# Optimization experiments

Measured on AMD Instinct MI355X. Metric: run time of the kernel, lower is better.

## Reference

```python
import jax, jax.numpy as jnp
import numpy as np
from jax import lax

DN = ('NCHW', 'OIHW', 'NCHW')
DENSITY = 0.1  # fraction of active pillar sites


def conv(x, w, stride=1):
    return lax.conv_general_dilated(x, w, (stride, stride), ((1, 1), (1, 1)), dimension_numbers=DN)


def bn(x, s, t):
    # inference-mode BN folded into per-channel scale/shift
    return x * s[None, :, None, None] + t[None, :, None, None]


def subm(x, w, s, t, mask):
    # submanifold sparse conv == dense conv on zero-filled grid, outputs kept only at active sites
    return bn(conv(x, w), s, t) * mask


def basic_block(x, mask, w, s, t):
    # Sparse2DBasicBlock: relu(bn(conv)) -> bn(conv) -> add identity -> relu
    out = jax.nn.relu(subm(x, w[0], s[0], t[0], mask))
    out = subm(out, w[1], s[1], t[1], mask)
    return jax.nn.relu(out + x)


def downsample_mask(m):
    # regular sparse conv (k=3, s=2, p=1): output active iff any input in window active
    return lax.reduce_window(m, 0.0, lax.max, (1, 1, 3, 3), (1, 1, 2, 2), ((0, 0), (0, 0), (1, 1), (1, 1)))


def down_stage(x, m_in, wd, w, s, t):
    m = downsample_mask(m_in)
    h = jax.nn.relu(bn(conv(x, wd, 2), s[0], t[0]) * m)
    h = basic_block(h, m, w[0:2], s[1:3], t[1:3])
    h = basic_block(h, m, w[2:4], s[3:5], t[3:5])
    return h, m


def forward_all(x, mask, w1, s1, t1, wd2, w2, s2, t2, wd3, w3, s3, t3, wd4, w4, s4, t4, w5, s5, t5):
    x = x * mask
    # conv1: Sparse2DBasicBlockV (conv0 + block) + Sparse2DBasicBlock
    h = jax.nn.relu(subm(x, w1[0], s1[0], t1[0], mask))
    h = basic_block(h, mask, w1[1:3], s1[1:3], t1[1:3])
    x1 = basic_block(h, mask, w1[3:5], s1[3:5], t1[3:5])
    x2, m2 = down_stage(x1, mask, wd2, w2, s2, t2)
    x3, m3 = down_stage(x2, m2, wd3, w3, s3, t3)
    x4, m4 = down_stage(x3, m3, wd4, w4, s4, t4)
    # conv5: dense stage on x_conv4.dense()
    h = jax.nn.relu(bn(conv(x4, w5[0], 2), s5[0], t5[0]))
    h = jax.nn.relu(bn(conv(h, w5[1]), s5[1], t5[1]))
    x5 = jax.nn.relu(bn(conv(h, w5[2]), s5[2], t5[2]))
    return x1, x2, x3, x4, x5


def setup_inputs() -> dict:
    key = jax.random.key(0)
    ks = jax.random.split(key, 16)
    B, C, H, W = 2, 32, 512, 512

    def mkw(k, o, i, n=None):
        shape = (o, i, 3, 3) if n is None else (n, o, i, 3, 3)
        return jax.random.normal(k, shape, jnp.float32) * float(np.sqrt(2.0 / (i * 9)))

    def sb(k, n, c):
        k1, k2 = jax.random.split(k)
        return (1.0 + 0.1 * jax.random.normal(k1, (n, c), jnp.float32),
                0.05 * jax.random.normal(k2, (n, c), jnp.float32))

    x = jax.random.normal(ks[0], (B, C, H, W), jnp.float32)
    mask_p = jax.random.uniform(ks[1], (B, 1, H, W), jnp.float32)
    w1 = mkw(ks[2], 32, 32, 5); s1, t1 = sb(ks[3], 5, 32)
    wd2 = mkw(ks[4], 64, 32); w2 = mkw(ks[5], 64, 64, 4); s2, t2 = sb(ks[6], 5, 64)
    wd3 = mkw(ks[7], 128, 64); w3 = mkw(ks[8], 128, 128, 4); s3, t3 = sb(ks[9], 5, 128)
    wd4 = mkw(ks[10], 256, 128); w4 = mkw(ks[11], 256, 256, 4); s4, t4 = sb(ks[12], 5, 256)
    w5 = mkw(ks[13], 256, 256, 3); s5, t5 = sb(ks[14], 3, 256)
    return dict(x=x, mask_p=mask_p, w1=w1, s1=s1, t1=t1, wd2=wd2, w2=w2, s2=s2, t2=t2,
                wd3=wd3, w3=w3, s3=s3, t3=t3, wd4=wd4, w4=w4, s4=s4, t4=t4,
                w5=w5, s5=s5, t5=t5)


def reference(x, mask_p, w1, s1, t1, wd2, w2, s2, t2, wd3, w3, s3, t3, wd4, w4, s4, t4, w5, s5, t5):
    mask = (mask_p < DENSITY).astype(x.dtype)
    return forward_all(x, mask, w1, s1, t1, wd2, w2, s2, t2, wd3, w3, s3, t3, wd4, w4, s4, t4, w5, s5, t5)
```

## Files before the change

### kernel.cpp

```cpp
#include <hip/hip_runtime.h>

typedef __attribute__((ext_vector_type(8))) _Float16 f16x8;
typedef __attribute__((ext_vector_type(4))) _Float16 f16x4;
typedef __attribute__((ext_vector_type(4))) float f32x4;

__global__ void mask_make(const float* __restrict__ x, const float* __restrict__ mp,
                          float* __restrict__ m, _Float16* __restrict__ x0,
                          int* __restrict__ act, int* __restrict__ cnt,
                          int B, int HW) {
    int i = blockIdx.x * blockDim.x + threadIdx.x;
    const int tid = threadIdx.x;
    const int lane = tid & 63;
    const int wv = tid >> 6;
    bool active = (mp[i] < 0.1f);
    float mv = active ? 1.0f : 0.0f;
    m[i] = mv;
    int b = i / HW, p = i - b * HW;
    const float* xb = x + ((size_t)b * 32) * HW + p;
    _Float16* ob = x0 + (size_t)i * 32;
    #pragma unroll
    for (int c = 0; c < 32; ++c) ob[c] = (_Float16)(xb[(size_t)c * HW] * mv);

    __shared__ int wcnt[4];
    __shared__ int bbase;
    unsigned long long ball = __ballot(active);
    int wtot = __popcll(ball);
    int prefix = __popcll(ball & ((1ull << lane) - 1ull));
    if (lane == 0) wcnt[wv] = wtot;
    __syncthreads();
    if (tid == 0) {
        int s = 0;
        #pragma unroll
        for (int w = 0; w < 4; ++w) { int tv = wcnt[w]; wcnt[w] = s; s += tv; }
        bbase = (s > 0) ? atomicAdd(&cnt[b], s) : 0;
    }
    __syncthreads();
    if (active) act[b * HW + bbase + wcnt[wv] + prefix] = p;
}

__global__ void mask_down(const float* __restrict__ mi, float* __restrict__ mo,
                          int B, int Hi, int Wi, int Ho, int Wo) {
    int i = blockIdx.x * blockDim.x + threadIdx.x;
    if (i >= B * Ho * Wo) return;
    int wo = i % Wo;
    int t = i / Wo;
    int ho = t % Ho;
    int b = t / Ho;
    float v = 0.0f;
    #pragma unroll
    for (int kh = 0; kh < 3; ++kh) {
        int hi = ho * 2 + kh - 1;
        if (hi < 0 || hi >= Hi) continue;
        #pragma unroll
        for (int kw = 0; kw < 3; ++kw) {
            int wi = wo * 2 + kw - 1;
            if (wi < 0 || wi >= Wi) continue;
            v = fmaxf(v, mi[((size_t)b * Hi + hi) * Wi + wi]);
        }
    }
    mo[i] = v;
}

struct WSeg { const float* src; int cin, cout, ck, cum; };
struct WArgs { WSeg seg[23]; int total; };

__global__ void reorder_all(WArgs A, _Float16* __restrict__ rw) {
    int idx = blockIdx.x * 256 + threadIdx.x;
    if (idx >= A.total) return;
    int s = 0;
    #pragma unroll
    for (int k = 1; k < 23; ++k) if (idx >= A.seg[k].cum) s = k;
    WSeg g = A.seg[s];
    int local = idx - g.cum;
    int kk = local % g.ck;
    int t2 = local / g.ck;
    int co = t2 % g.cout;
    int chunk = t2 / g.cout;
    int chunkc = g.cin / g.ck;
    int tap = chunk / chunkc, cc = chunk - tap * chunkc;
    int ci = cc * g.ck + kk;
    rw[g.cum + local] = (_Float16)g.src[((size_t)co * g.cin + ci) * 9 + tap];
}

template<int BM, int BN, int CK>
__global__ __launch_bounds__(256, 4)
void conv_mfma(const _Float16* __restrict__ in, const _Float16* __restrict__ rw,
               const float* __restrict__ s, const float* __restrict__ t,
               const float* __restrict__ mask, const _Float16* __restrict__ res,
               float* __restrict__ out32, _Float16* __restrict__ out16,
               int Cin, int Cout, int Hin, int Win, int Hout, int Wout,
               int TH, int TW, int stride, int relu)
{
    constexpr int WM = (BM >= 64) ? BM / 2 : BM;
    constexpr int WAVES_M = BM / WM;
    constexpr int WAVES_N = 4 / WAVES_M;
    constexpr int WN = BN / WAVES_N;
    constexpr int MR = WM / 16;
    constexpr int NR = WN / 16;
    constexpr int KH = CK / 32;
    constexpr int ELEMS = (CK * BN) / 256;
    constexpr int NV = ELEMS / 8;
    constexpr int TPP = 256 / BN;
    constexpr int LDST = CK + 8;

    __shared__ _Float16 Bsm[2][BN * LDST];

    const int tid = threadIdx.x;
    const int lane = tid & 63;
    const int wv = tid >> 6;
    const int wm = wv / WAVES_N;
    const int wn = wv % WAVES_N;
    const int row = lane & 15, q = lane >> 4;

    const int tilesX = Wout / TW;
    const int oy0 = (blockIdx.x / tilesX) * TH;
    const int ox0 = (blockIdx.x % tilesX) * TW;
    const int co0 = blockIdx.y * BM;
    const int b = blockIdx.z;

    const int HWin = Hin * Win;
    const int HWo = Hout * Wout;
    const int cicn = Cin >> 5;
    const int cocn = Cout >> 5;
    const int chunkc = Cin / CK;
    const int nIter = 9 * chunkc;

    const int sn = tid / TPP;
    const int kb = (tid % TPP) * ELEMS;
    const int sty = sn / TW;
    const int stx = sn - sty * TW;
    const int soy = oy0 + sty;
    const int sox = ox0 + stx;

    f32x4 acc[MR][NR];
    #pragma unroll
    for (int m = 0; m < MR; ++m)
        #pragma unroll
        for (int n = 0; n < NR; ++n)
            #pragma unroll
            for (int r = 0; r < 4; ++r) acc[m][n][r] = 0.0f;

    auto LOADG = [&](int c, f16x8* dst) {
        int tap = c / chunkc, cc = c - tap * chunkc;
        int iy = soy * stride + (tap / 3) - 1;
        int ix = sox * stride + (tap - (tap / 3) * 3) - 1;
        bool ok = (iy >= 0 && iy < Hin && ix >= 0 && ix < Win);
        size_t pixoff = (size_t)iy * Win + ix;
        #pragma unroll
        for (int i = 0; i < NV; ++i) {
            int k = kb + 8 * i;
            const _Float16* p = in +
                (((size_t)(b * cicn + cc * KH + (k >> 5)) * HWin + pixoff) << 5) + (k & 31);
            dst[i] = ok ? *(const f16x8*)p : f16x8{};
        }
    };
    auto LOADW = [&](int c, f16x8 (&dst)[KH][MR]) {
        #pragma unroll
        for (int m = 0; m < MR; ++m) {
            int co = co0 + wm * WM + m * 16 + row;
            const _Float16* ap = rw + ((size_t)c * Cout + co) * CK + (q << 3);
            #pragma unroll
            for (int h = 0; h < KH; ++h) dst[h][m] = *(const f16x8*)(ap + 32 * h);
        }
    };
    auto WLDS = [&](int buf, const f16x8* v) {
        #pragma unroll
        for (int i = 0; i < NV; ++i)
            *(f16x8*)&Bsm[buf][sn * LDST + kb + 8 * i] = v[i];
    };
    auto DO_CHUNK = [&](const _Float16* bp, f16x8 (&awx)[KH][MR]) {
        f16x8 bh[KH][NR];
        #pragma unroll
        for (int n = 0; n < NR; ++n) {
            int nl = wn * WN + n * 16 + row;
            const _Float16* bb = bp + nl * LDST + (q << 3);
            #pragma unroll
            for (int h = 0; h < KH; ++h) bh[h][n] = *(const f16x8*)(bb + 32 * h);
        }
        #pragma unroll
        for (int h = 0; h < KH; ++h)
            #pragma unroll
            for (int m = 0; m < MR; ++m)
                #pragma unroll
                for (int n = 0; n < NR; ++n)
                    acc[m][n] = __builtin_amdgcn_mfma_f32_16x16x32_f16(awx[h][m], bh[h][n], acc[m][n], 0, 0, 0);
    };

    f16x8 awA[KH][MR], awB[KH][MR];
    f16x8 v[NV];
    LOADG(0, v);
    LOADW(0, awA);
    WLDS(0, v);
    __syncthreads();

    for (int c = 0; c < nIter; c += 2) {
        f16x8 v2[NV];
        bool h1 = (c + 1) < nIter;
        if (h1) { LOADG(c + 1, v2); LOADW(c + 1, awB); }
        DO_CHUNK(&Bsm[0][0], awA);
        if (h1) WLDS(1, v2);
        __syncthreads();
        if (!h1) break;
        f16x8 v3[NV];
        bool h2 = (c + 2) < nIter;
        if (h2) { LOADG(c + 2, v3); LOADW(c + 2, awA); }
        DO_CHUNK(&Bsm[1][0], awB);
        if (h2) WLDS(0, v3);
        __syncthreads();
    }

    int pix[NR]; float mv[NR];
    #pragma unroll
    for (int n = 0; n < NR; ++n) {
        int nl = wn * WN + n * 16 + row;
        int ty = nl / TW, tx = nl - ty * TW;
        pix[n] = (oy0 + ty) * Wout + (ox0 + tx);
        mv[n] = mask ? mask[(size_t)b * HWo + pix[n]] : 1.0f;
    }
    #pragma unroll
    for (int m = 0; m < MR; ++m) {
        int cb = co0 + wm * WM + m * 16 + q * 4;
        float sc[4], sh[4];
        #pragma unroll
        for (int r = 0; r < 4; ++r) { sc[r] = s[cb + r]; sh[r] = t[cb + r]; }
        #pragma unroll
        for (int n = 0; n < NR; ++n) {
            size_t boff = ((size_t)(b * cocn + (cb >> 5)) * HWo + pix[n]) * 32 + (cb & 31);
            float val[4];
            #pragma unroll
            for (int r = 0; r < 4; ++r) val[r] = (acc[m][n][r] * sc[r] + sh[r]) * mv[n];
            if (res) {
                f16x4 rv = *(const f16x4*)&res[boff];
                #pragma unroll
                for (int r = 0; r < 4; ++r) val[r] += (float)rv[r];
            }
            if (relu) {
                #pragma unroll
                for (int r = 0; r < 4; ++r) val[r] = fmaxf(val[r], 0.0f);
            }
            if (out16) {
                f16x4 pk;
                #pragma unroll
                for (int r = 0; r < 4; ++r) pk[r] = (_Float16)val[r];
                *(f16x4*)&out16[boff] = pk;
            }
            if (out32) {
                #pragma unroll
                for (int r = 0; r < 4; ++r)
                    out32[((size_t)b * Cout + cb + r) * HWo + pix[n]] = val[r];
            }
        }
    }
}

__global__ __launch_bounds__(256, 4)
void conv_sparse(const _Float16* __restrict__ in, const _Float16* __restrict__ rw,
                 const float* __restrict__ s, const float* __restrict__ t,
                 const int* __restrict__ act, const int* __restrict__ cnt,
                 const _Float16* __restrict__ res,
                 float* __restrict__ out32, _Float16* __restrict__ out16,
                 int Hin, int Win, int relu)
{
    const int tid = threadIdx.x;
    const int lane = tid & 63;
    const int wv = tid >> 6;
    const int row = lane & 15, q = lane >> 4;
    const int b = blockIdx.z;
    const int HW = Hin * Win;
    const int nb = cnt[b];
    const int base = (blockIdx.x * 4 + wv) * 16;
    if (base >= nb) return;

    const int* actb = act + b * HW;
    const _Float16* inb = in + ((size_t)b * HW << 5);

    int j = base + row;
    bool vn = j < nb;
    int pn = vn ? actb[j] : 0;
    int py = pn / Win, px = pn - py * Win;

    f32x4 acc0, acc1;
    #pragma unroll
    for (int r = 0; r < 4; ++r) { acc0[r] = 0.0f; acc1[r] = 0.0f; }

    #pragma unroll
    for (int c = 0; c < 9; ++c) {
        const int dy = c / 3 - 1, dx = c - (c / 3) * 3 - 1;
        f16x8 a0 = *(const f16x8*)(rw + ((size_t)c * 32 + row) * 32 + (q << 3));
        f16x8 a1 = *(const f16x8*)(rw + ((size_t)c * 32 + 16 + row) * 32 + (q << 3));
        int iy = py + dy, ix = px + dx;
        bool ok = vn && iy >= 0 && iy < Hin && ix >= 0 && ix < Win;
        f16x8 bf = ok ? *(const f16x8*)(inb + ((size_t)(iy * Win + ix) << 5) + (q << 3))
                      : f16x8{};
        acc0 = __builtin_amdgcn_mfma_f32_16x16x32_f16(a0, bf, acc0, 0, 0, 0);
        acc1 = __builtin_amdgcn_mfma_f32_16x16x32_f16(a1, bf, acc1, 0, 0, 0);
    }

    if (!vn) return;
    size_t pbase = ((size_t)b * HW + pn) << 5;
    #pragma unroll
    for (int m = 0; m < 2; ++m) {
        const f32x4& am = m ? acc1 : acc0;
        int cb = m * 16 + q * 4;
        float val[4];
        #pragma unroll
        for (int r = 0; r < 4; ++r) val[r] = am[r] * s[cb + r] + t[cb + r];
        if (res) {
            f16x4 rv = *(const f16x4*)&res[pbase + cb];
            #pragma unroll
            for (int r = 0; r < 4; ++r) val[r] += (float)rv[r];
        }
        if (relu) {
            #pragma unroll
            for (int r = 0; r < 4; ++r) val[r] = fmaxf(val[r], 0.0f);
        }
        f16x4 pk;
        #pragma unroll
        for (int r = 0; r < 4; ++r) pk[r] = (_Float16)val[r];
        *(f16x4*)&out16[pbase + cb] = pk;
        if (out32) {
            #pragma unroll
            for (int r = 0; r < 4; ++r)
                out32[((size_t)(b * 32 + cb + r)) * HW + pn] = val[r];
        }
    }
}

extern "C" void kernel_launch(void* const* d_in, const int* in_sizes, int n_in,
                              void* d_out, int out_size, void* d_ws, size_t ws_size,
                              hipStream_t stream) {
    const int B = 2;

    const float* x      = (const float*)d_in[0];
    const float* mask_p = (const float*)d_in[1];
    const float* w1  = (const float*)d_in[2];
    const float* s1  = (const float*)d_in[3];
    const float* t1  = (const float*)d_in[4];
    const float* wd2 = (const float*)d_in[5];
    const float* w2  = (const float*)d_in[6];
    const float* s2  = (const float*)d_in[7];
    const float* t2  = (const float*)d_in[8];
    const float* wd3 = (const float*)d_in[9];
    const float* w3  = (const float*)d_in[10];
    const float* s3  = (const float*)d_in[11];
    const float* t3  = (const float*)d_in[12];
    const float* wd4 = (const float*)d_in[13];
    const float* w4  = (const float*)d_in[14];
    const float* s4  = (const float*)d_in[15];
    const float* t4  = (const float*)d_in[16];
    const float* w5  = (const float*)d_in[17];
    const float* s5  = (const float*)d_in[18];
    const float* t5  = (const float*)d_in[19];

    float* x1o = (float*)d_out;
    float* x2o = x1o + 16777216;
    float* x3o = x2o + 8388608;
    float* x4o = x3o + 4194304;
    float* x5o = x4o + 2097152;

    _Float16* rwbase = (_Float16*)d_ws;
    float* m1 = (float*)d_ws + 2649600;
    float* m2 = m1 + 524288;
    float* m3 = m2 + 131072;
    float* m4 = m3 + 32768;
    int* act  = (int*)(m4 + 8192);
    int* cnt  = act + 524288;
    _Float16* P = (_Float16*)(cnt + 32);
    _Float16* Q = P + 16777216;
    _Float16* R = Q + 16777216;

    WArgs wa;
    int cum = 0, si = 0;
    const _Float16* rp[23];
    auto addseg = [&](const float* src, int cin, int cout, int ck) {
        wa.seg[si].src = src; wa.seg[si].cin = cin; wa.seg[si].cout = cout;
        wa.seg[si].ck = ck; wa.seg[si].cum = cum;
        rp[si] = rwbase + cum;
        cum += cout * cin * 9; si++;
    };
    for (int i = 0; i < 5; ++i) addseg(w1 + (size_t)i * 9216, 32, 32, 32);
    addseg(wd2, 32, 64, 32);
    for (int i = 0; i < 4; ++i) addseg(w2 + (size_t)i * 36864, 64, 64, 64);
    addseg(wd3, 64, 128, 64);
    for (int i = 0; i < 4; ++i) addseg(w3 + (size_t)i * 147456, 128, 128, 64);
    addseg(wd4, 128, 256, 64);
    for (int i = 0; i < 4; ++i) addseg(w4 + (size_t)i * 589824, 256, 256, 64);
    for (int i = 0; i < 3; ++i) addseg(w5 + (size_t)i * 589824, 256, 256, 64);
    wa.total = cum;
    reorder_all<<<(cum + 255) / 256, 256, 0, stream>>>(wa, rwbase);

    hipMemsetAsync(cnt, 0, 2 * sizeof(int), stream);
    hipMemsetAsync(Q, 0, 16777216 * sizeof(_Float16), stream);
    hipMemsetAsync(R, 0, 16777216 * sizeof(_Float16), stream);
    hipMemsetAsync(x1o, 0, 16777216 * sizeof(float), stream);

    {
        int n = B * 512 * 512;
        mask_make<<<(n + 255) / 256, 256, 0, stream>>>(x, mask_p, m1, P, act, cnt, B, 512 * 512);
        mask_down<<<(B * 256 * 256 + 255) / 256, 256, 0, stream>>>(m1, m2, B, 512, 512, 256, 256);
        mask_down<<<(B * 128 * 128 + 255) / 256, 256, 0, stream>>>(m2, m3, B, 256, 256, 128, 128);
        mask_down<<<(B * 64 * 64 + 255) / 256, 256, 0, stream>>>(m3, m4, B, 128, 128, 64, 64);
    }

    auto conv = [&](const _Float16* in, const _Float16* rwp, const float* sp, const float* tp,
                    const float* mk, const _Float16* rs, float* o32, _Float16* o16,
                    int Cin, int Cout, int Hin, int Win, int stride, int CK) {
        int Hout = Hin / stride, Wout = Win / stride, HWo = Hout * Wout;
        int TW = (Wout < 64) ? Wout : 64;
        int TH = 64 / TW;
        dim3 grid(HWo / 64, Cout / 64, B);
        if (CK == 32)
            conv_mfma<64, 64, 32><<<grid, 256, 0, stream>>>(in, rwp, sp, tp, mk, rs, o32, o16,
                Cin, Cout, Hin, Win, Hout, Wout, TH, TW, stride, 1);
        else
            conv_mfma<64, 64, 64><<<grid, 256, 0, stream>>>(in, rwp, sp, tp, mk, rs, o32, o16,
                Cin, Cout, Hin, Win, Hout, Wout, TH, TW, stride, 1);
    };
    auto sconv = [&](const _Float16* in, const _Float16* rwp, const float* sp, const float* tp,
                     const _Float16* rs, float* o32, _Float16* o16) {
        dim3 grid(1024, 1, B);
        conv_sparse<<<grid, 256, 0, stream>>>(in, rwp, sp, tp, act, cnt, rs, o32, o16, 512, 512, 1);
    };

    sconv(P, rp[0], s1 + 0,   t1 + 0,   nullptr, nullptr, Q);
    sconv(Q, rp[1], s1 + 32,  t1 + 32,  nullptr, nullptr, R);
    sconv(R, rp[2], s1 + 64,  t1 + 64,  Q,       nullptr, P);
    sconv(P, rp[3], s1 + 96,  t1 + 96,  nullptr, nullptr, Q);
    sconv(Q, rp[4], s1 + 128, t1 + 128, P,       x1o,     R);

    conv(R, rp[5], s2 + 0,   t2 + 0,   m2, nullptr, nullptr, P, 32, 64, 512, 512, 2, 32);
    conv(P, rp[6], s2 + 64,  t2 + 64,  m2, nullptr, nullptr, Q, 64, 64, 256, 256, 1, 64);
    conv(Q, rp[7], s2 + 128, t2 + 128, m2, P,       nullptr, P, 64, 64, 256, 256, 1, 64);
    conv(P, rp[8], s2 + 192, t2 + 192, m2, nullptr, nullptr, Q, 64, 64, 256, 256, 1, 64);
    conv(Q, rp[9], s2 + 256, t2 + 256, m2, P,       x2o,     P, 64, 64, 256, 256, 1, 64);

    conv(P, rp[10], s3 + 0,   t3 + 0,   m3, nullptr, nullptr, Q, 64, 128, 256, 256, 2, 64);
    conv(Q, rp[11], s3 + 128, t3 + 128, m3, nullptr, nullptr, R, 128, 128, 128, 128, 1, 64);
    conv(R, rp[12], s3 + 256, t3 + 256, m3, Q,       nullptr, Q, 128, 128, 128, 128, 1, 64);
    conv(Q, rp[13], s3 + 384, t3 + 384, m3, nullptr, nullptr, R, 128, 128, 128, 128, 1, 64);
    conv(R, rp[14], s3 + 512, t3 + 512, m3, Q,       x3o,     Q, 128, 128, 128, 128, 1, 64);

    conv(Q, rp[15], s4 + 0,    t4 + 0,    m4, nullptr, nullptr, P, 128, 256, 128, 128, 2, 64);
    conv(P, rp[16], s4 + 256,  t4 + 256,  m4, nullptr, nullptr, R, 256, 256, 64, 64, 1, 64);
    conv(R, rp[17], s4 + 512,  t4 + 512,  m4, P,       nullptr, P, 256, 256, 64, 64, 1, 64);
    conv(P, rp[18], s4 + 768,  t4 + 768,  m4, nullptr, nullptr, R, 256, 256, 64, 64, 1, 64);
    conv(R, rp[19], s4 + 1024, t4 + 1024, m4, P,       x4o,     P, 256, 256, 64, 64, 1, 64);

    conv(P, rp[20], s5 + 0,   t5 + 0,   nullptr, nullptr, nullptr, Q, 256, 256, 64, 64, 2, 64);
    conv(Q, rp[21], s5 + 256, t5 + 256, nullptr, nullptr, nullptr, R, 256, 256, 32, 32, 1, 64);
    conv(R, rp[22], s5 + 512, t5 + 512, nullptr, nullptr, x5o, nullptr, 256, 256, 32, 32, 1, 64);
}
```

Before: 1.087 ms.

## Deepen conv prefetch pipeline, use narrower pixel tiles for deep stages, merge memsets

The dense MFMA conv main loop now prefetches global input two chunks ahead into register buffers and issues the weight loads after each chunk's MFMAs, so memory latency overlaps more compute. Stages 4 and 5 (64x64 and 32x32 grids, 256 channels) use a 64x32 tile instead of 64x64, doubling block count to fill more CUs on small spatial layers. The two scratch-buffer memsets are merged into one, which assumes Q and R are contiguous. The extra register buffers raise VGPR pressure and may reduce occupancy.

```diff
diff --git a/kernel.cpp b/kernel.cpp
--- a/kernel.cpp
+++ b/kernel.cpp
@@ -91,9 +91,8 @@
                int Cin, int Cout, int Hin, int Win, int Hout, int Wout,
                int TH, int TW, int stride, int relu)
 {
-    constexpr int WM = (BM >= 64) ? BM / 2 : BM;
-    constexpr int WAVES_M = BM / WM;
-    constexpr int WAVES_N = 4 / WAVES_M;
+    constexpr int WM = BM / 2;
+    constexpr int WAVES_N = 2;
     constexpr int WN = BN / WAVES_N;
     constexpr int MR = WM / 16;
     constexpr int NR = WN / 16;
@@ -108,8 +107,8 @@
     const int tid = threadIdx.x;
     const int lane = tid & 63;
     const int wv = tid >> 6;
-    const int wm = wv / WAVES_N;
-    const int wn = wv % WAVES_N;
+    const int wm = wv >> 1;
+    const int wn = wv & 1;
     const int row = lane & 15, q = lane >> 4;
 
     const int tilesX = Wout / TW;
@@ -187,25 +186,25 @@
     };
 
     f16x8 awA[KH][MR], awB[KH][MR];
-    f16x8 v[NV];
-    LOADG(0, v);
+    f16x8 vA[NV], vB[NV];
+    LOADG(0, vA);
     LOADW(0, awA);
-    WLDS(0, v);
+    WLDS(0, vA);
+    if (1 < nIter) { LOADG(1, vB); LOADW(1, awB); }
     __syncthreads();
 
     for (int c = 0; c < nIter; c += 2) {
-        f16x8 v2[NV];
-        bool h1 = (c + 1) < nIter;
-        if (h1) { LOADG(c + 1, v2); LOADW(c + 1, awB); }
+        bool n1 = (c + 1) < nIter, n2 = (c + 2) < nIter, n3 = (c + 3) < nIter;
+        if (n2) LOADG(c + 2, vA);
         DO_CHUNK(&Bsm[0][0], awA);
-        if (h1) WLDS(1, v2);
+        if (n2) LOADW(c + 2, awA);
+        if (n1) WLDS(1, vB);
         __syncthreads();
-        if (!h1) break;
-        f16x8 v3[NV];
-        bool h2 = (c + 2) < nIter;
-        if (h2) { LOADG(c + 2, v3); LOADW(c + 2, awA); }
+        if (!n1) break;
+        if (n3) LOADG(c + 3, vB);
         DO_CHUNK(&Bsm[1][0], awB);
-        if (h2) WLDS(0, v3);
+        if (n3) LOADW(c + 3, awB);
+        if (n2) WLDS(0, vA);
         __syncthreads();
     }
 
@@ -390,8 +389,7 @@
     reorder_all<<<(cum + 255) / 256, 256, 0, stream>>>(wa, rwbase);
 
     hipMemsetAsync(cnt, 0, 2 * sizeof(int), stream);
-    hipMemsetAsync(Q, 0, 16777216 * sizeof(_Float16), stream);
-    hipMemsetAsync(R, 0, 16777216 * sizeof(_Float16), stream);
+    hipMemsetAsync(Q, 0, 2 * 16777216 * sizeof(_Float16), stream);
     hipMemsetAsync(x1o, 0, 16777216 * sizeof(float), stream);
 
     {
@@ -404,16 +402,19 @@
 
     auto conv = [&](const _Float16* in, const _Float16* rwp, const float* sp, const float* tp,
                     const float* mk, const _Float16* rs, float* o32, _Float16* o16,
-                    int Cin, int Cout, int Hin, int Win, int stride, int CK) {
+                    int Cin, int Cout, int Hin, int Win, int stride, int CK, int BN) {
         int Hout = Hin / stride, Wout = Win / stride, HWo = Hout * Wout;
-        int TW = (Wout < 64) ? Wout : 64;
-        int TH = 64 / TW;
-        dim3 grid(HWo / 64, Cout / 64, B);
+        int TW = (Wout < BN) ? Wout : BN;
+        int TH = BN / TW;
+        dim3 grid(HWo / BN, Cout / 64, B);
         if (CK == 32)
             conv_mfma<64, 64, 32><<<grid, 256, 0, stream>>>(in, rwp, sp, tp, mk, rs, o32, o16,
                 Cin, Cout, Hin, Win, Hout, Wout, TH, TW, stride, 1);
+        else if (BN == 64)
+            conv_mfma<64, 64, 64><<<grid, 256, 0, stream>>>(in, rwp, sp, tp, mk, rs, o32, o16,
+                Cin, Cout, Hin, Win, Hout, Wout, TH, TW, stride, 1);
         else
-            conv_mfma<64, 64, 64><<<grid, 256, 0, stream>>>(in, rwp, sp, tp, mk, rs, o32, o16,
+            conv_mfma<64, 32, 64><<<grid, 256, 0, stream>>>(in, rwp, sp, tp, mk, rs, o32, o16,
                 Cin, Cout, Hin, Win, Hout, Wout, TH, TW, stride, 1);
     };
     auto sconv = [&](const _Float16* in, const _Float16* rwp, const float* sp, const float* tp,
@@ -428,25 +429,25 @@
     sconv(P, rp[3], s1 + 96,  t1 + 96,  nullptr, nullptr, Q);
     sconv(Q, rp[4], s1 + 128, t1 + 128, P,       x1o,     R);
 
-    conv(R, rp[5], s2 + 0,   t2 + 0,   m2, nullptr, nullptr, P, 32, 64, 512, 512, 2, 32);
-    conv(P, rp[6], s2 + 64,  t2 + 64,  m2, nullptr, nullptr, Q, 64, 64, 256, 256, 1, 64);
-    conv(Q, rp[7], s2 + 128, t2 + 128, m2, P,       nullptr, P, 64, 64, 256, 256, 1, 64);
-    conv(P, rp[8], s2 + 192, t2 + 192, m2, nullptr, nullptr, Q, 64, 64, 256, 256, 1, 64);
-    conv(Q, rp[9], s2 + 256, t2 + 256, m2, P,       x2o,     P, 64, 64, 256, 256, 1, 64);
-
-    conv(P, rp[10], s3 + 0,   t3 + 0,   m3, nullptr, nullptr, Q, 64, 128, 256, 256, 2, 64);
-    conv(Q, rp[11], s3 + 128, t3 + 128, m3, nullptr, nullptr, R, 128, 128, 128, 128, 1, 64);
-    conv(R, rp[12], s3 + 256, t3 + 256, m3, Q,       nullptr, Q, 128, 128, 128, 128, 1, 64);
-    conv(Q, rp[13], s3 + 384, t3 + 384, m3, nullptr, nullptr, R, 128, 128, 128, 128, 1, 64);
-    conv(R, rp[14], s3 + 512, t3 + 512, m3, Q,       x3o,     Q, 128, 128, 128, 128, 1, 64);
-
-    conv(Q, rp[15], s4 + 0,    t4 + 0,    m4, nullptr, nullptr, P, 128, 256, 128, 128, 2, 64);
-    conv(P, rp[16], s4 + 256,  t4 + 256,  m4, nullptr, nullptr, R, 256, 256, 64, 64, 1, 64);
-    conv(R, rp[17], s4 + 512,  t4 + 512,  m4, P,       nullptr, P, 256, 256, 64, 64, 1, 64);
-    conv(P, rp[18], s4 + 768,  t4 + 768,  m4, nullptr, nullptr, R, 256, 256, 64, 64, 1, 64);
-    conv(R, rp[19], s4 + 1024, t4 + 1024, m4, P,       x4o,     P, 256, 256, 64, 64, 1, 64);
-
-    conv(P, rp[20], s5 + 0,   t5 + 0,   nullptr, nullptr, nullptr, Q, 256, 256, 64, 64, 2, 64);
-    conv(Q, rp[21], s5 + 256, t5 + 256, nullptr, nullptr, nullptr, R, 256, 256, 32, 32, 1, 64);
-    conv(R, rp[22], s5 + 512, t5 + 512, nullptr, nullptr, x5o, nullptr, 256, 256, 32, 32, 1, 64);
-}
+    conv(R, rp[5], s2 + 0,   t2 + 0,   m2, nullptr, nullptr, P, 32, 64, 512, 512, 2, 32, 64);
+    conv(P, rp[6], s2 + 64,  t2 + 64,  m2, nullptr, nullptr, Q, 64, 64, 256, 256, 1, 64, 64);
+    conv(Q, rp[7], s2 + 128, t2 + 128, m2, P,       nullptr, P, 64, 64, 256, 256, 1, 64, 64);
+    conv(P, rp[8], s2 + 192, t2 + 192, m2, nullptr, nullptr, Q, 64, 64, 256, 256, 1, 64, 64);
+    conv(Q, rp[9], s2 + 256, t2 + 256, m2, P,       x2o,     P, 64, 64, 256, 256, 1, 64, 64);
+
+    conv(P, rp[10], s3 + 0,   t3 + 0,   m3, nullptr, nullptr, Q, 64, 128, 256, 256, 2, 64, 64);
+    conv(Q, rp[11], s3 + 128, t3 + 128, m3, nullptr, nullptr, R, 128, 128, 128, 128, 1, 64, 64);
+    conv(R, rp[12], s3 + 256, t3 + 256, m3, Q,       nullptr, Q, 128, 128, 128, 128, 1, 64, 64);
+    conv(Q, rp[13], s3 + 384, t3 + 384, m3, nullptr, nullptr, R, 128, 128, 128, 128, 1, 64, 64);
+    conv(R, rp[14], s3 + 512, t3 + 512, m3, Q,       x3o,     Q, 128, 128, 128, 128, 1, 64, 64);
+
+    conv(Q, rp[15], s4 + 0,    t4 + 0,    m4, nullptr, nullptr, P, 128, 256, 128, 128, 2, 64, 32);
+    conv(P, rp[16], s4 + 256,  t4 + 256,  m4, nullptr, nullptr, R, 256, 256, 64, 64, 1, 64, 32);
+    conv(R, rp[17], s4 + 512,  t4 + 512,  m4, P,       nullptr, P, 256, 256, 64, 64, 1, 64, 32);
+    conv(P, rp[18], s4 + 768,  t4 + 768,  m4, nullptr, nullptr, R, 256, 256, 64, 64, 1, 64, 32);
+    conv(R, rp[19], s4 + 1024, t4 + 1024, m4, P,       x4o,     P, 256, 256, 64, 64, 1, 64, 32);
+
+    conv(P, rp[20], s5 + 0,   t5 + 0,   nullptr, nullptr, nullptr, Q, 256, 256, 64, 64, 2, 64, 32);
+    conv(Q, rp[21], s5 + 256, t5 + 256, nullptr, nullptr, nullptr, R, 256, 256, 32, 32, 1, 64, 32);
+    conv(R, rp[22], s5 + 512, t5 + 512, nullptr, nullptr, x5o, nullptr, 256, 256, 32, 32, 1, 64, 32);
+}
```

Measured after the change: 1.211 ms. +11.4%, slower.

## Add LDS-free per-wave conv kernel for low-resolution stages 4 and 5

Applied to the files above, without the earlier changes.

Adds conv_bf, where each wave computes a 16-pixel by 64-channel tile straight from global memory with register double-buffering and no shared memory or block barriers. It replaces the tiled LDS conv for the 64x64 and 32x32 stages, which launched few blocks. Weights for those layers are reordered with 32-channel chunks to match the new kernel's indexing. The goal is more waves and lower sync overhead on the small late stages, at the cost of redundant global/L2 reads of inputs and weights across waves. Two memsets are also merged into one and the conv_mfma wave mapping is hardcoded.

```diff
diff --git a/kernel.cpp b/kernel.cpp
--- a/kernel.cpp
+++ b/kernel.cpp
@@ -91,9 +91,8 @@
                int Cin, int Cout, int Hin, int Win, int Hout, int Wout,
                int TH, int TW, int stride, int relu)
 {
-    constexpr int WM = (BM >= 64) ? BM / 2 : BM;
-    constexpr int WAVES_M = BM / WM;
-    constexpr int WAVES_N = 4 / WAVES_M;
+    constexpr int WM = BM / 2;
+    constexpr int WAVES_N = 2;
     constexpr int WN = BN / WAVES_N;
     constexpr int MR = WM / 16;
     constexpr int NR = WN / 16;
@@ -108,8 +107,8 @@
     const int tid = threadIdx.x;
     const int lane = tid & 63;
     const int wv = tid >> 6;
-    const int wm = wv / WAVES_N;
-    const int wn = wv % WAVES_N;
+    const int wm = wv >> 1;
+    const int wn = wv & 1;
     const int row = lane & 15, q = lane >> 4;
 
     const int tilesX = Wout / TW;
@@ -254,6 +253,100 @@
 }
 
 __global__ __launch_bounds__(256, 4)
+void conv_bf(const _Float16* __restrict__ in, const _Float16* __restrict__ rw,
+             const float* __restrict__ s, const float* __restrict__ t,
+             const float* __restrict__ mask, const _Float16* __restrict__ res,
+             float* __restrict__ out32, _Float16* __restrict__ out16,
+             int Cin, int Cout, int Hin, int Win, int Hout, int Wout,
+             int stride, int relu)
+{
+    const int lane = threadIdx.x & 63;
+    const int wv = threadIdx.x >> 6;
+    const int row = lane & 15, q = lane >> 4;
+    const int b = blockIdx.z;
+    const int HWo = Hout * Wout;
+    const int ntile = HWo >> 4;
+    const int gw = blockIdx.x * 4 + wv;
+    const int tile = gw % ntile;
+    const int cog = gw / ntile;
+    const int co0 = cog * 64;
+    const int HWin = Hin * Win;
+    const int cicn = Cin >> 5;
+    const int cocn = Cout >> 5;
+    const int nIter = 9 * cicn;
+
+    const int pix = tile * 16 + row;
+    const int py = pix / Wout, px_ = pix - py * Wout;
+    const int iy0 = py * stride - 1, ix0 = px_ * stride - 1;
+    const _Float16* inb = in + (((size_t)b * cicn) * HWin << 5);
+
+    f32x4 acc[4];
+    #pragma unroll
+    for (int m = 0; m < 4; ++m)
+        #pragma unroll
+        for (int r = 0; r < 4; ++r) acc[m][r] = 0.0f;
+
+    auto LOADB = [&](int c, f16x8& dst) {
+        int tap = c / cicn, cc = c - tap * cicn;
+        int iy = iy0 + tap / 3, ix = ix0 + tap - (tap / 3) * 3;
+        bool ok = (iy >= 0 && iy < Hin && ix >= 0 && ix < Win);
+        dst = ok ? *(const f16x8*)(inb + (((size_t)cc * HWin + (size_t)iy * Win + ix) << 5) + (q << 3))
+                 : f16x8{};
+    };
+    auto LOADA = [&](int c, f16x8 (&dst)[4]) {
+        const _Float16* ap = rw + ((size_t)c * Cout + co0 + row) * 32 + (q << 3);
+        #pragma unroll
+        for (int m = 0; m < 4; ++m) dst[m] = *(const f16x8*)(ap + (size_t)m * 512);
+    };
+
+    f16x8 aA[4], aB[4], bfA, bfB;
+    LOADB(0, bfA); LOADA(0, aA);
+    for (int c = 0; c < nIter; c += 2) {
+        bool h1 = (c + 1) < nIter, h2 = (c + 2) < nIter;
+        if (h1) { LOADB(c + 1, bfB); LOADA(c + 1, aB); }
+        #pragma unroll
+        for (int m = 0; m < 4; ++m)
+            acc[m] = __builtin_amdgcn_mfma_f32_16x16x32_f16(aA[m], bfA, acc[m], 0, 0, 0);
+        if (h2) { LOADB(c + 2, bfA); LOADA(c + 2, aA); }
+        if (h1) {
+            #pragma unroll
+            for (int m = 0; m < 4; ++m)
+                acc[m] = __builtin_amdgcn_mfma_f32_16x16x32_f16(aB[m], bfB, acc[m], 0, 0, 0);
+        }
+    }
+
+    float mv = mask ? mask[(size_t)b * HWo + pix] : 1.0f;
+    #pragma unroll
+    for (int m = 0; m < 4; ++m) {
+        int cb = co0 + m * 16 + q * 4;
+        size_t boff = ((size_t)(b * cocn + (cb >> 5)) * HWo + pix) * 32 + (cb & 31);
+        float val[4];
+        #pragma unroll
+        for (int r = 0; r < 4; ++r) val[r] = (acc[m][r] * s[cb + r] + t[cb + r]) * mv;
+        if (res) {
+            f16x4 rv = *(const f16x4*)&res[boff];
+            #pragma unroll
+            for (int r = 0; r < 4; ++r) val[r] += (float)rv[r];
+        }
+        if (relu) {
+            #pragma unroll
+            for (int r = 0; r < 4; ++r) val[r] = fmaxf(val[r], 0.0f);
+        }
+        if (out16) {
+            f16x4 pk;
+            #pragma unroll
+            for (int r = 0; r < 4; ++r) pk[r] = (_Float16)val[r];
+            *(f16x4*)&out16[boff] = pk;
+        }
+        if (out32) {
+            #pragma unroll
+            for (int r = 0; r < 4; ++r)
+                out32[((size_t)b * Cout + cb + r) * HWo + pix] = val[r];
+        }
+    }
+}
+
+__global__ __launch_bounds__(256, 4)
 void conv_sparse(const _Float16* __restrict__ in, const _Float16* __restrict__ rw,
                  const float* __restrict__ s, const float* __restrict__ t,
                  const int* __restrict__ act, const int* __restrict__ cnt,
@@ -383,15 +476,14 @@
     for (int i = 0; i < 4; ++i) addseg(w2 + (size_t)i * 36864, 64, 64, 64);
     addseg(wd3, 64, 128, 64);
     for (int i = 0; i < 4; ++i) addseg(w3 + (size_t)i * 147456, 128, 128, 64);
-    addseg(wd4, 128, 256, 64);
-    for (int i = 0; i < 4; ++i) addseg(w4 + (size_t)i * 589824, 256, 256, 64);
-    for (int i = 0; i < 3; ++i) addseg(w5 + (size_t)i * 589824, 256, 256, 64);
+    addseg(wd4, 128, 256, 32);
+    for (int i = 0; i < 4; ++i) addseg(w4 + (size_t)i * 589824, 256, 256, 32);
+    for (int i = 0; i < 3; ++i) addseg(w5 + (size_t)i * 589824, 256, 256, 32);
     wa.total = cum;
     reorder_all<<<(cum + 255) / 256, 256, 0, stream>>>(wa, rwbase);
 
     hipMemsetAsync(cnt, 0, 2 * sizeof(int), stream);
-    hipMemsetAsync(Q, 0, 16777216 * sizeof(_Float16), stream);
-    hipMemsetAsync(R, 0, 16777216 * sizeof(_Float16), stream);
+    hipMemsetAsync(Q, 0, 2 * 16777216 * sizeof(_Float16), stream);
     hipMemsetAsync(x1o, 0, 16777216 * sizeof(float), stream);
 
     {
@@ -416,6 +508,15 @@
             conv_mfma<64, 64, 64><<<grid, 256, 0, stream>>>(in, rwp, sp, tp, mk, rs, o32, o16,
                 Cin, Cout, Hin, Win, Hout, Wout, TH, TW, stride, 1);
     };
+    auto bconv = [&](const _Float16* in, const _Float16* rwp, const float* sp, const float* tp,
+                     const float* mk, const _Float16* rs, float* o32, _Float16* o16,
+                     int Cin, int Cout, int Hin, int Win, int stride) {
+        int Hout = Hin / stride, Wout = Win / stride, HWo = Hout * Wout;
+        int waves = (HWo / 16) * (Cout / 64);
+        dim3 grid(waves / 4, 1, B);
+        conv_bf<<<grid, 256, 0, stream>>>(in, rwp, sp, tp, mk, rs, o32, o16,
+            Cin, Cout, Hin, Win, Hout, Wout, stride, 1);
+    };
     auto sconv = [&](const _Float16* in, const _Float16* rwp, const float* sp, const float* tp,
                      const _Float16* rs, float* o32, _Float16* o16) {
         dim3 grid(1024, 1, B);
@@ -440,13 +541,13 @@
     conv(Q, rp[13], s3 + 384, t3 + 384, m3, nullptr, nullptr, R, 128, 128, 128, 128, 1, 64);
     conv(R, rp[14], s3 + 512, t3 + 512, m3, Q,       x3o,     Q, 128, 128, 128, 128, 1, 64);
 
-    conv(Q, rp[15], s4 + 0,    t4 + 0,    m4, nullptr, nullptr, P, 128, 256, 128, 128, 2, 64);
-    conv(P, rp[16], s4 + 256,  t4 + 256,  m4, nullptr, nullptr, R, 256, 256, 64, 64, 1, 64);
-    conv(R, rp[17], s4 + 512,  t4 + 512,  m4, P,       nullptr, P, 256, 256, 64, 64, 1, 64);
-    conv(P, rp[18], s4 + 768,  t4 + 768,  m4, nullptr, nullptr, R, 256, 256, 64, 64, 1, 64);
-    conv(R, rp[19], s4 + 1024, t4 + 1024, m4, P,       x4o,     P, 256, 256, 64, 64, 1, 64);
-
-    conv(P, rp[20], s5 + 0,   t5 + 0,   nullptr, nullptr, nullptr, Q, 256, 256, 64, 64, 2, 64);
-    conv(Q, rp[21], s5 + 256, t5 + 256, nullptr, nullptr, nullptr, R, 256, 256, 32, 32, 1, 64);
-    conv(R, rp[22], s5 + 512, t5 + 512, nullptr, nullptr, x5o, nullptr, 256, 256, 32, 32, 1, 64);
-}
+    bconv(Q, rp[15], s4 + 0,    t4 + 0,    m4, nullptr, nullptr, P, 128, 256, 128, 128, 2);
+    bconv(P, rp[16], s4 + 256,  t4 + 256,  m4, nullptr, nullptr, R, 256, 256, 64, 64, 1);
+    bconv(R, rp[17], s4 + 512,  t4 + 512,  m4, P,       nullptr, P, 256, 256, 64, 64, 1);
+    bconv(P, rp[18], s4 + 768,  t4 + 768,  m4, nullptr, nullptr, R, 256, 256, 64, 64, 1);
+    bconv(R, rp[19], s4 + 1024, t4 + 1024, m4, P,       x4o,     P, 256, 256, 64, 64, 1);
+
+    bconv(P, rp[20], s5 + 0,   t5 + 0,   nullptr, nullptr, nullptr, Q, 256, 256, 64, 64, 2);
+    bconv(Q, rp[21], s5 + 256, t5 + 256, nullptr, nullptr, nullptr, R, 256, 256, 32, 32, 1);
+    bconv(R, rp[22], s5 + 512, t5 + 512, nullptr, nullptr, x5o, nullptr, 256, 256, 32, 32, 1);
+}
```

Measured after the change: 1.086 ms. Within noise of the previous version (-0.1%).
